# Kernel optimization log

Measured on AMD Instinct MI355X. Metric: run time of the kernel, lower is better.

The kernel has to match this reference:

```python
import jax, jax.numpy as jnp
import numpy as np

LN_EPS = 1e-5
SM_EPS = 1e-16  # torch_geometric softmax denominator eps


def _layernorm(x, g, b):
    mu = jnp.mean(x, axis=-1, keepdims=True)
    var = jnp.var(x, axis=-1, keepdims=True)
    return (x - mu) * jax.lax.rsqrt(var + LN_EPS) * g + b


def setup_inputs() -> dict:
    d = 128
    L = 3
    N = 50000
    E = 800000
    key = jax.random.key(0)
    ks = jax.random.split(key, 16)
    s = 1.0 / np.sqrt(d)
    inp = {
        "edge_index": jax.random.randint(ks[0], (2, E), 0, N, dtype=jnp.int32),
        "x": jax.random.normal(ks[1], (N, d), dtype=jnp.float32),
        # per-layer attention params, stacked over layers
        "Wq": jax.random.uniform(ks[2], (L, d, d), jnp.float32, -s, s),
        "bq": jax.random.uniform(ks[3], (L, d), jnp.float32, -s, s),
        "Wk": jax.random.uniform(ks[4], (L, d, d), jnp.float32, -s, s),
        "bk": jax.random.uniform(ks[5], (L, d), jnp.float32, -s, s),
        "Wv": jax.random.uniform(ks[6], (L, d, d), jnp.float32, -s, s),
        "bv": jax.random.uniform(ks[7], (L, d), jnp.float32, -s, s),
        "ln_g": jnp.ones((L, d), jnp.float32),
        "ln_b": jnp.zeros((L, d), jnp.float32),
        # MLP stack: d -> 4d -> 2d -> d (no activations, per source)
        "W1": jax.random.uniform(ks[8], (4 * d, d), jnp.float32, -s, s),
        "b1": jax.random.uniform(ks[9], (4 * d,), jnp.float32, -s, s),
        "W2": jax.random.uniform(ks[10], (2 * d, 4 * d), jnp.float32, -0.5 * s, 0.5 * s),
        "b2": jax.random.uniform(ks[11], (2 * d,), jnp.float32, -0.5 * s, 0.5 * s),
        "W3": jax.random.uniform(ks[12], (d, 2 * d), jnp.float32, -0.7 * s, 0.7 * s),
        "b3": jax.random.uniform(ks[13], (d,), jnp.float32, -0.7 * s, 0.7 * s),
        "Wvec": jax.random.uniform(ks[14], (1, d), jnp.float32, -s, s),
        "bvec": jax.random.uniform(ks[15], (1,), jnp.float32, -s, s),
        "fn_g": jnp.ones((d,), jnp.float32),
        "fn_b": jnp.zeros((d,), jnp.float32),
    }
    return inp


def reference(edge_index, x, Wq, bq, Wk, bk, Wv, bv, ln_g, ln_b,
              W1, b1, W2, b2, W3, b3, Wvec, bvec, fn_g, fn_b):
    N = x.shape[0]
    src = edge_index[0]
    dst = edge_index[1]
    x_i = x[src]  # [E, d]
    x_j = x[dst]  # [E, d]
    L = Wq.shape[0]
    attn_output = None
    query = None
    for i in range(L):
        q = x_i @ Wq[i].T + bq[i]
        k = x_j @ Wk[i].T + bk[i]
        v = x_j @ Wv[i].T + bv[i]
        alpha = jnp.sum(q * k, axis=-1)  # [E]
        # segment softmax over destination node (torch_geometric.utils.softmax)
        m = jax.ops.segment_max(alpha, dst, num_segments=N)
        e = jnp.exp(alpha - m[dst])
        s = jax.ops.segment_sum(e, dst, num_segments=N)
        alpha = e / (s[dst] + SM_EPS)
        attn_output = jax.nn.relu(alpha[:, None] * v)  # dropout = identity (eval)
        query = _layernorm(x_j + attn_output, ln_g[i], ln_b[i])
    adj = attn_output  # squeeze(0) is a no-op for [E, d]
    adj = adj @ W1.T + b1
    adj = adj @ W2.T + b2
    adj = adj @ W3.T + b3
    adj = _layernorm(adj + query, fn_g, fn_b)
    adj_logits = (adj @ Wvec.T + bvec)[:, 0]  # [E]
    return adj_logits
```

## Files before the change

kernel.cpp:

```cpp
#include <hip/hip_runtime.h>


typedef __attribute__((ext_vector_type(8))) short bf16x8;
typedef __attribute__((ext_vector_type(4))) float f32x4;

__device__ __forceinline__ unsigned short f2bf(float f) {
  unsigned int u = __float_as_uint(f);
  unsigned int r = (u + 0x7fffu + ((u >> 16) & 1u)) >> 16;
  return (unsigned short)r;
}
__device__ __forceinline__ float blo(unsigned int u) {
  return __uint_as_float(u << 16);
}
__device__ __forceinline__ float bhi(unsigned int u) {
  return __uint_as_float(u & 0xffff0000u);
}

__global__ __launch_bounds__(128) void k_TW(
    const float* __restrict__ W2, const float* __restrict__ W1,
    const float* __restrict__ Wq, const float* __restrict__ Wk,
    const float* __restrict__ Wv, float* __restrict__ T,
    unsigned short* __restrict__ Wqb, unsigned short* __restrict__ Wkb,
    unsigned short* __restrict__ Wvb, float* __restrict__ sArr, int N) {
  const int b = blockIdx.x, t = threadIdx.x;
  if (b < 256) {
    float acc = 0.f;
    for (int k = 0; k < 512; ++k) acc += W2[b * 512 + k] * W1[k * 128 + t];
    T[b * 128 + t] = acc;
  } else if (b < 640) {
    const int idx = (b - 256) * 128 + t;
    const int m = idx >> 14, i = idx & 16383;
    const float* s = (m == 0) ? Wq : (m == 1) ? Wk : Wv;
    unsigned short* d = (m == 0) ? Wqb : (m == 1) ? Wkb : Wvb;
    d[i] = f2bf(s[i]);
  } else {
    const int i = (b - 640) * 128 + t;
    if (i < N) sArr[i] = 0.f;
  }
}

__global__ __launch_bounds__(256) void k_Ac(
    const float* __restrict__ W3, const float* __restrict__ T,
    const float* __restrict__ W2, const float* __restrict__ b1,
    const float* __restrict__ b2, const float* __restrict__ b3,
    const float* __restrict__ g, const float* __restrict__ lb,
    const float* __restrict__ fg, const float* __restrict__ fb,
    const float* __restrict__ wv, unsigned short* __restrict__ A3b,
    float* __restrict__ cfull, float* __restrict__ C) {
  __shared__ float t1[256];
  __shared__ float cf[128];
  const int b = blockIdx.x, t = threadIdx.x;
  if (b < 64) {
    const int i = 2 * b + (t >> 7), j = t & 127;
    float acc = 0.f;
    for (int k = 0; k < 256; ++k) acc += W3[i * 256 + k] * T[k * 128 + j];
    A3b[i * 128 + j] = f2bf(acc);
    return;
  }
  float acc = b2[t];
  for (int c = 0; c < 512; ++c) acc += W2[t * 512 + c] * b1[c];
  t1[t] = acc;
  __syncthreads();
  if (t < 128) {
    float a = b3[t];
    for (int k = 0; k < 256; ++k) a += W3[t * 256 + k] * t1[k];
    cfull[t] = a;
    cf[t] = a;
  }
  __syncthreads();
  if (t < 64) {
    const int l = t;
    const float2 gv = ((const float2*)g)[l];
    const float2 bv = ((const float2*)lb)[l];
    const float2 fgv = ((const float2*)fg)[l];
    const float2 fbv = ((const float2*)fb)[l];
    const float2 wvv = ((const float2*)wv)[l];
    const float P0 = cf[2 * l] + bv.x, P1 = cf[2 * l + 1] + bv.y;
    const float w0 = fgv.x * wvv.x, w1 = fgv.y * wvv.y;
    float s[9];
    s[0] = P0 + P1;
    s[1] = P0 * w0 + P1 * w1;
    s[2] = P0 * P0 + P1 * P1;
    s[3] = gv.x + gv.y;
    s[4] = gv.x * w0 + gv.y * w1;
    s[5] = gv.x * gv.x + gv.y * gv.y;
    s[6] = P0 * gv.x + P1 * gv.y;
    s[7] = w0 + w1;
    s[8] = fbv.x * wvv.x + fbv.y * wvv.y;
#pragma unroll
    for (int m = 32; m >= 1; m >>= 1)
#pragma unroll
      for (int i = 0; i < 9; ++i) s[i] += __shfl_xor(s[i], m, 64);
    if (l == 0)
#pragma unroll
      for (int i = 0; i < 9; ++i) C[i] = s[i];
  }
}

__device__ __forceinline__ void qk_pass(const unsigned short* __restrict__ Wb,
                                        const float* __restrict__ bias,
                                        unsigned short* __restrict__ outB,
                                        const bf16x8* af, int nb, int wv16,
                                        int ln, int g4, int N) {
#pragma unroll
  for (int cb = 0; cb < 8; ++cb) {
    f32x4 acc = {0.f, 0.f, 0.f, 0.f};
#pragma unroll
    for (int kb = 0; kb < 4; ++kb) {
      const bf16x8 bfr =
          *(const bf16x8*)(Wb + ((cb * 16 + ln) << 7) + kb * 32 + g4 * 8);
      acc = __builtin_amdgcn_mfma_f32_16x16x32_bf16(af[kb], bfr, acc, 0, 0, 0);
    }
    const int col = cb * 16 + ln;
    const float bs = bias[col];
#pragma unroll
    for (int r = 0; r < 4; ++r) {
      const int lr = wv16 + g4 * 4 + r;
      if (nb + lr < N) outB[(size_t)(nb + lr) * 128 + col] = f2bf(acc[r] + bs);
    }
  }
}

__global__ __launch_bounds__(256) void k_node(
    const float* __restrict__ x, const unsigned short* __restrict__ Wqb,
    const unsigned short* __restrict__ Wkb,
    const unsigned short* __restrict__ Wvb,
    const unsigned short* __restrict__ A3b, const float* __restrict__ bq,
    const float* __restrict__ bk, const float* __restrict__ bv,
    const float* __restrict__ cfull, const float* __restrict__ g,
    const float* __restrict__ lb, const float* __restrict__ fg,
    const float* __restrict__ wvp, unsigned short* __restrict__ Qb,
    unsigned short* __restrict__ Kb, float* __restrict__ S, int N) {
  __shared__ float xf[64][132];
  __shared__ unsigned short uls[64][136];
  __shared__ float cg[128], cw[128], cP[128];
  const int t = threadIdx.x;
  const int nb = blockIdx.x * 64;
  if (t < 128) {
    cg[t] = g[t];
    cw[t] = fg[t] * wvp[t];
    cP[t] = cfull[t] + lb[t];
  }
  for (int i = t; i < 64 * 32; i += 256) {
    const int j = i >> 5, c4 = i & 31;
    const int n = nb + j;
    float4 v = make_float4(0.f, 0.f, 0.f, 0.f);
    if (n < N) v = ((const float4*)x)[(size_t)n * 32 + c4];
    *(float4*)&xf[j][c4 * 4] = v;
  }
  __syncthreads();
  const int wv16 = __builtin_amdgcn_readfirstlane(t >> 6) * 16;
  const int l = t & 63;
  const int ln = l & 15, g4 = l >> 4;

  bf16x8 af[4];
#pragma unroll
  for (int kb = 0; kb < 4; ++kb) {
    const float* p = &xf[wv16 + ln][kb * 32 + g4 * 8];
    const float4 a0 = *(const float4*)p;
    const float4 a1 = *(const float4*)(p + 4);
    bf16x8 r;
    r[0] = (short)f2bf(a0.x); r[1] = (short)f2bf(a0.y);
    r[2] = (short)f2bf(a0.z); r[3] = (short)f2bf(a0.w);
    r[4] = (short)f2bf(a1.x); r[5] = (short)f2bf(a1.y);
    r[6] = (short)f2bf(a1.z); r[7] = (short)f2bf(a1.w);
    af[kb] = r;
  }

  qk_pass(Wqb, bq, Qb, af, nb, wv16, ln, g4, N);
  qk_pass(Wkb, bk, Kb, af, nb, wv16, ln, g4, N);

  float uf[8][4];
#pragma unroll
  for (int cb = 0; cb < 8; ++cb) {
    f32x4 acc = {0.f, 0.f, 0.f, 0.f};
#pragma unroll
    for (int kb = 0; kb < 4; ++kb) {
      const bf16x8 bfr =
          *(const bf16x8*)(Wvb + ((cb * 16 + ln) << 7) + kb * 32 + g4 * 8);
      acc = __builtin_amdgcn_mfma_f32_16x16x32_bf16(af[kb], bfr, acc, 0, 0, 0);
    }
    const int col = cb * 16 + ln;
    const float bs = bv[col];
#pragma unroll
    for (int r = 0; r < 4; ++r) {
      const float v = fmaxf(acc[r] + bs, 0.f);
      uf[cb][r] = v;
      uls[wv16 + g4 * 4 + r][col] = f2bf(v);
    }
  }

  bf16x8 af2[4];
#pragma unroll
  for (int kb = 0; kb < 4; ++kb)
    af2[kb] = *(const bf16x8*)&uls[wv16 + ln][kb * 32 + g4 * 8];
  float vmf[8][4];
#pragma unroll
  for (int cb = 0; cb < 8; ++cb) {
    f32x4 acc = {0.f, 0.f, 0.f, 0.f};
#pragma unroll
    for (int kb = 0; kb < 4; ++kb) {
      const bf16x8 bfr =
          *(const bf16x8*)(A3b + ((cb * 16 + ln) << 7) + kb * 32 + g4 * 8);
      acc = __builtin_amdgcn_mfma_f32_16x16x32_bf16(af2[kb], bfr, acc, 0, 0, 0);
    }
#pragma unroll
    for (int r = 0; r < 4; ++r) vmf[cb][r] = acc[r];
  }

  float gc[8], wc[8], Pc[8];
#pragma unroll
  for (int cb = 0; cb < 8; ++cb) {
    const int col = cb * 16 + ln;
    gc[cb] = cg[col];
    wc[cb] = cw[col];
    Pc[cb] = cP[col];
  }

#pragma unroll
  for (int r = 0; r < 4; ++r) {
    const int row = wv16 + g4 * 4 + r;
    float s[23];
#pragma unroll
    for (int i = 0; i < 23; ++i) s[i] = 0.f;
#pragma unroll
    for (int cb = 0; cb < 8; ++cb) {
      const float xv = xf[row][cb * 16 + ln];
      const float u = uf[cb][r];
      const float v = vmf[cb][r];
      const float gg = gc[cb], ww = wc[cb], PP = Pc[cb];
      const float xg = xv * gg, ug = u * gg;
      s[0] += xv;
      s[1] += u;
      s[2] += xv * xv;
      s[3] += xv * u;
      s[4] += u * u;
      s[5] += v;
      s[6] += v * ww;
      s[7] += xg;
      s[8] += ug;
      s[9] += xg * ww;
      s[10] += ug * ww;
      s[11] += PP * v;
      s[12] += v * v;
      s[13] += PP * xg;
      s[14] += PP * ug;
      s[15] += v * xg;
      s[16] += v * ug;
      s[17] += v * gg;
      s[18] += xg * xg;
      s[19] += xg * ug;
      s[20] += ug * ug;
      s[21] += xg * gg;
      s[22] += ug * gg;
    }
#pragma unroll
    for (int m = 1; m <= 8; m <<= 1)
#pragma unroll
      for (int i = 0; i < 23; ++i) s[i] += __shfl_xor(s[i], m, 64);
    const int n2 = nb + row;
    if (ln == 0 && n2 < N) {
      float* o = S + (size_t)n2 * 24;
      o[0] = s[0] * (1.f / 128.f);
      o[1] = s[1] * (1.f / 128.f);
#pragma unroll
      for (int i = 2; i < 23; ++i) o[i] = s[i];
      o[23] = 0.f;
    }
  }
}

__global__ __launch_bounds__(256) void k_edge_alpha(
    const int* __restrict__ ei, const unsigned short* __restrict__ Qb,
    const unsigned short* __restrict__ Kb, float* __restrict__ eArr,
    float* __restrict__ sArr, int E) {
  const int t = threadIdx.x;
  const int l = t & 15;
  const int e = blockIdx.x * 16 + (t >> 4);
  if (e >= E) return;
  const int src = ei[e];
  const int dst = ei[E + e];
  const uint4 qv = ((const uint4*)Qb)[(size_t)src * 16 + l];
  const uint4 kv = ((const uint4*)Kb)[(size_t)dst * 16 + l];
  float p = blo(qv.x) * blo(kv.x);
  p = fmaf(bhi(qv.x), bhi(kv.x), p);
  p = fmaf(blo(qv.y), blo(kv.y), p);
  p = fmaf(bhi(qv.y), bhi(kv.y), p);
  p = fmaf(blo(qv.z), blo(kv.z), p);
  p = fmaf(bhi(qv.z), bhi(kv.z), p);
  p = fmaf(blo(qv.w), blo(kv.w), p);
  p = fmaf(bhi(qv.w), bhi(kv.w), p);
#pragma unroll
  for (int m = 8; m >= 1; m >>= 1) p += __shfl_xor(p, m, 16);
  if (l == 0) {
    const float ex = __expf(p);
    eArr[e] = ex;
    atomicAdd(&sArr[dst], ex);
  }
}

__global__ __launch_bounds__(256) void k_edge_out(
    const int* __restrict__ ei, const float* __restrict__ eArr,
    const float* __restrict__ sArr, const float* __restrict__ S,
    const float* __restrict__ C, const float* __restrict__ bvec,
    float* __restrict__ out, int E) {
  const int e = blockIdx.x * 256 + threadIdx.x;
  if (e >= E) return;
  const int dst = ei[E + e];
  const float t = eArr[e] / (sArr[dst] + 1e-16f);
  const float4* o = (const float4*)(S + (size_t)dst * 24);
  const float4 q0 = o[0], q1 = o[1], q2 = o[2], q3 = o[3], q4 = o[4],
               q5 = o[5];
  const float mx = q0.x, mU = q0.y, sxx = q0.z, sxu = q0.w;
  const float suu = q1.x, sv = q1.y, svw = q1.z, sxg = q1.w;
  const float sug = q2.x, sxgw = q2.y, sugw = q2.z, spv = q2.w;
  const float svv = q3.x, pxg = q3.y, pug = q3.z, vxg = q3.w;
  const float vug = q4.x, vg = q4.y, xgxg = q4.z, xgug = q4.w;
  const float ugug = q5.x, xgg = q5.y, ugg = q5.z;
  const float SP = C[0], SPw = C[1], SPP = C[2], SG = C[3], SGw = C[4],
              GG = C[5], SPG = C[6], Sw = C[7], s0 = C[8];
  const float mu = mx + t * mU;
  const float qy = (sxx + 2.f * t * sxu + t * t * suu) * (1.f / 128.f);
  const float i1 = rsqrtf(qy - mu * mu + 1e-5f);
  const float sz = SP + t * sv + i1 * (sxg + t * sug - mu * SG);
  const float szw = SPw + t * svw + i1 * (sxgw + t * sugw - mu * SGw);
  const float cross = pxg + t * (pug + vxg) + t * t * vug - mu * (SPG + t * vg);
  const float rr = xgxg + 2.f * t * xgug + t * t * ugug -
                   2.f * mu * (xgg + t * ugg) + mu * mu * GG;
  const float szz =
      SPP + 2.f * t * spv + t * t * svv + 2.f * i1 * cross + i1 * i1 * rr;
  const float muz = sz * (1.f / 128.f);
  const float varz = szz * (1.f / 128.f) - muz * muz;
  const float iz = rsqrtf(varz + 1e-5f);
  out[e] = iz * (szw - muz * Sw) + s0 + bvec[0];
}

extern "C" void kernel_launch(void* const* d_in, const int* in_sizes, int n_in,
                              void* d_out, int out_size, void* d_ws,
                              size_t ws_size, hipStream_t stream) {
  const int* ei = (const int*)d_in[0];
  const float* x = (const float*)d_in[1];
  const float* Wq = (const float*)d_in[2];
  const float* bq = (const float*)d_in[3];
  const float* Wk = (const float*)d_in[4];
  const float* bk = (const float*)d_in[5];
  const float* Wv = (const float*)d_in[6];
  const float* bv = (const float*)d_in[7];
  const float* ln_g = (const float*)d_in[8];
  const float* ln_b = (const float*)d_in[9];
  const float* W1 = (const float*)d_in[10];
  const float* b1 = (const float*)d_in[11];
  const float* W2 = (const float*)d_in[12];
  const float* b2 = (const float*)d_in[13];
  const float* W3 = (const float*)d_in[14];
  const float* b3 = (const float*)d_in[15];
  const float* Wvec = (const float*)d_in[16];
  const float* bvec = (const float*)d_in[17];
  const float* fn_g = (const float*)d_in[18];
  const float* fn_b = (const float*)d_in[19];

  const int E = in_sizes[0] / 2;
  const int N = in_sizes[1] / 128;

  const float* Wq2 = Wq + 2 * 128 * 128;
  const float* bq2 = bq + 2 * 128;
  const float* Wk2 = Wk + 2 * 128 * 128;
  const float* bk2 = bk + 2 * 128;
  const float* Wv2 = Wv + 2 * 128 * 128;
  const float* bv2 = bv + 2 * 128;
  const float* g2 = ln_g + 2 * 128;
  const float* lb2 = ln_b + 2 * 128;

  float* ws = (float*)d_ws;
  float* T = ws;
  float* cfull = T + 32768;
  float* consts = cfull + 128;
  unsigned short* Wqb = (unsigned short*)(consts + 16);
  unsigned short* Wkb = Wqb + 16384;
  unsigned short* Wvb = Wkb + 16384;
  unsigned short* A3b = Wvb + 16384;
  float* fbase = consts + 16 + 32768;
  unsigned short* Qb = (unsigned short*)fbase;
  unsigned short* Kb = Qb + (size_t)N * 128;
  float* S = fbase + (size_t)N * 128;
  float* eArr = S + (size_t)N * 24;
  float* sArr = eArr + E;

  const int zblk = (N + 127) / 128;
  k_TW<<<640 + zblk, 128, 0, stream>>>(W2, W1, Wq2, Wk2, Wv2, T, Wqb, Wkb,
                                       Wvb, sArr, N);
  k_Ac<<<65, 256, 0, stream>>>(W3, T, W2, b1, b2, b3, g2, lb2, fn_g, fn_b,
                               Wvec, A3b, cfull, consts);

  const int nblk = (N + 63) / 64;
  k_node<<<nblk, 256, 0, stream>>>(x, Wqb, Wkb, Wvb, A3b, bq2, bk2, bv2,
                                   cfull, g2, lb2, fn_g, Wvec, Qb, Kb, S, N);
  const int ablk = (E + 15) / 16;
  k_edge_alpha<<<ablk, 256, 0, stream>>>(ei, Qb, Kb, eArr, sArr, E);
  const int oblk = (E + 255) / 256;
  k_edge_out<<<oblk, 256, 0, stream>>>(ei, eArr, sArr, S, consts, bvec,
                                       (float*)d_out, E);
}
```

Measured before the change: 220.0 us.

## Shrink node-kernel LDS to one bf16 tile and coalesce Q/K stores

Replaces the fp32 x tile, the separate u tile and the constant arrays with a single bf16 tile that is reused for x, Q, K and u, which cuts LDS per block and adds a launch-bounds occupancy hint. Q and K results are staged through the tile and written out as 16-byte row vectors instead of scattered 2-byte stores. In exchange, the fp32 x values needed for the statistics are re-read from global memory, and the per-column constants are loaded directly. The tile reuse relies on each wave touching only its own rows, so no extra barriers are added.

```diff
diff --git a/kernel.cpp b/kernel.cpp
--- a/kernel.cpp
+++ b/kernel.cpp
@@ -97,31 +97,7 @@
   }
 }
 
-__device__ __forceinline__ void qk_pass(const unsigned short* __restrict__ Wb,
-                                        const float* __restrict__ bias,
-                                        unsigned short* __restrict__ outB,
-                                        const bf16x8* af, int nb, int wv16,
-                                        int ln, int g4, int N) {
-#pragma unroll
-  for (int cb = 0; cb < 8; ++cb) {
-    f32x4 acc = {0.f, 0.f, 0.f, 0.f};
-#pragma unroll
-    for (int kb = 0; kb < 4; ++kb) {
-      const bf16x8 bfr =
-          *(const bf16x8*)(Wb + ((cb * 16 + ln) << 7) + kb * 32 + g4 * 8);
-      acc = __builtin_amdgcn_mfma_f32_16x16x32_bf16(af[kb], bfr, acc, 0, 0, 0);
-    }
-    const int col = cb * 16 + ln;
-    const float bs = bias[col];
-#pragma unroll
-    for (int r = 0; r < 4; ++r) {
-      const int lr = wv16 + g4 * 4 + r;
-      if (nb + lr < N) outB[(size_t)(nb + lr) * 128 + col] = f2bf(acc[r] + bs);
-    }
-  }
-}
-
-__global__ __launch_bounds__(256) void k_node(
+__global__ __launch_bounds__(256, 3) void k_node(
     const float* __restrict__ x, const unsigned short* __restrict__ Wqb,
     const unsigned short* __restrict__ Wkb,
     const unsigned short* __restrict__ Wvb,
@@ -131,44 +107,70 @@
     const float* __restrict__ lb, const float* __restrict__ fg,
     const float* __restrict__ wvp, unsigned short* __restrict__ Qb,
     unsigned short* __restrict__ Kb, float* __restrict__ S, int N) {
-  __shared__ float xf[64][132];
-  __shared__ unsigned short uls[64][136];
-  __shared__ float cg[128], cw[128], cP[128];
+  __shared__ unsigned short tile[64][136];
   const int t = threadIdx.x;
   const int nb = blockIdx.x * 64;
-  if (t < 128) {
-    cg[t] = g[t];
-    cw[t] = fg[t] * wvp[t];
-    cP[t] = cfull[t] + lb[t];
-  }
   for (int i = t; i < 64 * 32; i += 256) {
     const int j = i >> 5, c4 = i & 31;
     const int n = nb + j;
     float4 v = make_float4(0.f, 0.f, 0.f, 0.f);
     if (n < N) v = ((const float4*)x)[(size_t)n * 32 + c4];
-    *(float4*)&xf[j][c4 * 4] = v;
+    unsigned int lo = f2bf(v.x) | ((unsigned int)f2bf(v.y) << 16);
+    unsigned int hi = f2bf(v.z) | ((unsigned int)f2bf(v.w) << 16);
+    *(uint2*)&tile[j][c4 << 2] = make_uint2(lo, hi);
   }
   __syncthreads();
   const int wv16 = __builtin_amdgcn_readfirstlane(t >> 6) * 16;
   const int l = t & 63;
   const int ln = l & 15, g4 = l >> 4;
-
   bf16x8 af[4];
 #pragma unroll
-  for (int kb = 0; kb < 4; ++kb) {
-    const float* p = &xf[wv16 + ln][kb * 32 + g4 * 8];
-    const float4 a0 = *(const float4*)p;
-    const float4 a1 = *(const float4*)(p + 4);
-    bf16x8 r;
-    r[0] = (short)f2bf(a0.x); r[1] = (short)f2bf(a0.y);
-    r[2] = (short)f2bf(a0.z); r[3] = (short)f2bf(a0.w);
-    r[4] = (short)f2bf(a1.x); r[5] = (short)f2bf(a1.y);
-    r[6] = (short)f2bf(a1.z); r[7] = (short)f2bf(a1.w);
-    af[kb] = r;
-  }
-
-  qk_pass(Wqb, bq, Qb, af, nb, wv16, ln, g4, N);
-  qk_pass(Wkb, bk, Kb, af, nb, wv16, ln, g4, N);
+  for (int kb = 0; kb < 4; ++kb)
+    af[kb] = *(const bf16x8*)&tile[wv16 + ln][kb * 32 + g4 * 8];
+
+#pragma unroll
+  for (int cb = 0; cb < 8; ++cb) {
+    f32x4 acc = {0.f, 0.f, 0.f, 0.f};
+#pragma unroll
+    for (int kb = 0; kb < 4; ++kb) {
+      const bf16x8 bfr =
+          *(const bf16x8*)(Wqb + ((cb * 16 + ln) << 7) + kb * 32 + g4 * 8);
+      acc = __builtin_amdgcn_mfma_f32_16x16x32_bf16(af[kb], bfr, acc, 0, 0, 0);
+    }
+    const int col = cb * 16 + ln;
+    const float bs = bq[col];
+#pragma unroll
+    for (int r = 0; r < 4; ++r) tile[wv16 + g4 * 4 + r][col] = f2bf(acc[r] + bs);
+  }
+#pragma unroll
+  for (int c = 0; c < 4; ++c) {
+    const int row = wv16 + c * 4 + g4;
+    const int n = nb + row;
+    if (n < N)
+      ((uint4*)(Qb + (size_t)n * 128))[ln] = *(const uint4*)&tile[row][ln * 8];
+  }
+
+#pragma unroll
+  for (int cb = 0; cb < 8; ++cb) {
+    f32x4 acc = {0.f, 0.f, 0.f, 0.f};
+#pragma unroll
+    for (int kb = 0; kb < 4; ++kb) {
+      const bf16x8 bfr =
+          *(const bf16x8*)(Wkb + ((cb * 16 + ln) << 7) + kb * 32 + g4 * 8);
+      acc = __builtin_amdgcn_mfma_f32_16x16x32_bf16(af[kb], bfr, acc, 0, 0, 0);
+    }
+    const int col = cb * 16 + ln;
+    const float bs = bk[col];
+#pragma unroll
+    for (int r = 0; r < 4; ++r) tile[wv16 + g4 * 4 + r][col] = f2bf(acc[r] + bs);
+  }
+#pragma unroll
+  for (int c = 0; c < 4; ++c) {
+    const int row = wv16 + c * 4 + g4;
+    const int n = nb + row;
+    if (n < N)
+      ((uint4*)(Kb + (size_t)n * 128))[ln] = *(const uint4*)&tile[row][ln * 8];
+  }
 
   float uf[8][4];
 #pragma unroll
@@ -186,14 +188,14 @@
     for (int r = 0; r < 4; ++r) {
       const float v = fmaxf(acc[r] + bs, 0.f);
       uf[cb][r] = v;
-      uls[wv16 + g4 * 4 + r][col] = f2bf(v);
+      tile[wv16 + g4 * 4 + r][col] = f2bf(v);
     }
   }
 
   bf16x8 af2[4];
 #pragma unroll
   for (int kb = 0; kb < 4; ++kb)
-    af2[kb] = *(const bf16x8*)&uls[wv16 + ln][kb * 32 + g4 * 8];
+    af2[kb] = *(const bf16x8*)&tile[wv16 + ln][kb * 32 + g4 * 8];
   float vmf[8][4];
 #pragma unroll
   for (int cb = 0; cb < 8; ++cb) {
@@ -212,20 +214,21 @@
 #pragma unroll
   for (int cb = 0; cb < 8; ++cb) {
     const int col = cb * 16 + ln;
-    gc[cb] = cg[col];
-    wc[cb] = cw[col];
-    Pc[cb] = cP[col];
+    gc[cb] = g[col];
+    wc[cb] = fg[col] * wvp[col];
+    Pc[cb] = cfull[col] + lb[col];
   }
 
 #pragma unroll
   for (int r = 0; r < 4; ++r) {
     const int row = wv16 + g4 * 4 + r;
+    const int nrow = (nb + row < N) ? (nb + row) : (N - 1);
     float s[23];
 #pragma unroll
     for (int i = 0; i < 23; ++i) s[i] = 0.f;
 #pragma unroll
     for (int cb = 0; cb < 8; ++cb) {
-      const float xv = xf[row][cb * 16 + ln];
+      const float xv = x[(size_t)nrow * 128 + cb * 16 + ln];
       const float u = uf[cb][r];
       const float v = vmf[cb][r];
       const float gg = gc[cb], ww = wc[cb], PP = Pc[cb];
```

Result: no change. 221.9 us (+0.8%).
